# Kernel tuning notes

Hardware: AMD Instinct MI355X
Metric: run time of the kernel (lower is better)

## Reference

```python
import jax, jax.numpy as jnp
import numpy as np

N = 100000      # nodes
E = 1600000     # edges
F_IN = 512      # num_feat
HID = 128       # hidden dim (hardcoded in GNN)
ENC = 64        # encoder_dim
NCLS = 10       # num_classes
DOM = 40        # domain head hidden (hardcoded)


def setup_inputs() -> dict:
    key = jax.random.key(0)
    ks = jax.random.split(key, 16)
    def lin(k, fi, fo):
        kw, kb = jax.random.split(k)
        s = 1.0 / np.sqrt(fi)
        return (jax.random.uniform(kw, (fi, fo), jnp.float32, -s, s),
                jax.random.uniform(kb, (fo,), jnp.float32, -s, s))
    W1, b1 = lin(ks[0], F_IN, HID)
    W2, b2 = lin(ks[1], HID, ENC)
    att_w, att_b = lin(ks[2], ENC, 1)
    cls_w, cls_b = lin(ks[3], ENC, NCLS)
    dw1, db1 = lin(ks[4], ENC, DOM)
    dw2, db2 = lin(ks[5], DOM, 2)
    return {
        "x": jax.random.normal(ks[6], (N, F_IN), jnp.float32),
        "edge_index": jax.random.randint(ks[7], (2, E), 0, N, jnp.int64),
        "ppmi_edge_weight": jax.random.uniform(ks[8], (E,), jnp.float32, 0.01, 1.0),
        "rate": 1,
        "W1": W1, "b1": b1, "W2": W2, "b2": b2,
        "att_w": att_w, "att_b": att_b,
        "cls_w": cls_w, "cls_b": cls_b,
        "dw1": dw1, "db1": db1, "dw2": dw2, "db2": db2,
    }


def _edge_norm(src, dst, w):
    # symmetric normalization d^-1/2 * w * d^-1/2 (self-loops already included)
    deg = jax.ops.segment_sum(w, dst, num_segments=N)
    dinv = jnp.where(deg > 0, jax.lax.rsqrt(deg), 0.0)
    return dinv[src] * w * dinv[dst]


def _conv(h, W, b, src, dst, enorm):
    h = h @ W                                   # [N, out]
    msg = h[src] * enorm[:, None]               # [E+N, out] gather
    return jax.ops.segment_sum(msg, dst, num_segments=N) + b


def _encode(x, src, dst, enorm, W1, b1, W2, b2):
    h = jax.nn.relu(_conv(x, W1, b1, src, dst, enorm))  # dropout = identity (eval)
    return _conv(h, W2, b2, src, dst, enorm)


def reference(x, edge_index, ppmi_edge_weight, rate,
              W1, b1, W2, b2, att_w, att_b,
              cls_w, cls_b, dw1, db1, dw2, db2):
    loop = jnp.arange(N, dtype=edge_index.dtype)
    src = jnp.concatenate([edge_index[0], loop])
    dst = jnp.concatenate([edge_index[1], loop])
    ones_w = jnp.ones(src.shape[0], jnp.float32)
    ppmi_w = jnp.concatenate([ppmi_edge_weight, jnp.ones(N, jnp.float32)])

    gcn_norm = _edge_norm(src, dst, ones_w)
    ppmi_norm = _edge_norm(src, dst, ppmi_w)

    # both encoders share weights (base_model=self.encoder)
    g = _encode(x, src, dst, gcn_norm, W1, b1, W2, b2)    # [N, ENC]
    p = _encode(x, src, dst, ppmi_norm, W1, b1, W2, b2)   # [N, ENC]

    stacked = jnp.stack([g, p], axis=1)                   # [N, 2, ENC]
    logits = stacked @ att_w + att_b                      # [N, 2, 1]
    wts = jax.nn.softmax(logits, axis=1)
    emb = jnp.sum(stacked * wts, axis=1)                  # [N, ENC]

    class_predict = emb @ cls_w + cls_b
    r = jnp.float32(rate)
    # gradient reversal: identity fwd, -rate * grad bwd
    rev = jax.lax.stop_gradient((1.0 + r) * emb) - r * emb
    h = jax.nn.relu(rev @ dw1 + db1)                      # dropout = identity (eval)
    domain_predict = h @ dw2 + db2
    return emb, class_predict, domain_predict
```

## Files before the change

### kernel.cpp

```cpp
#include <hip/hip_runtime.h>
#include <math.h>
#include <stdint.h>

#define NND  100000
#define NED  1600000
#define FIN  512
#define HID  128
#define ENC  64
#define NCLS 10
#define DOM  40

#define SCAN_BS 256
#define NBS ((NND + SCAN_BS - 1) / SCAN_BS)

#define NGEMM 1563
#define NDEG  521
#define NPH1  (NGEMM + NDEG)

typedef __attribute__((ext_vector_type(8))) short short8v;
typedef __attribute__((ext_vector_type(8))) unsigned short ushort8v;
typedef __attribute__((ext_vector_type(4))) float f32x4;
typedef __attribute__((ext_vector_type(4))) unsigned int uint4v;


__device__ inline void split8(const float4 a, const float4 b,
                              short8v& hi, short8v& lo) {
  float f[8] = {a.x, a.y, a.z, a.w, b.x, b.y, b.z, b.w};
  uint4v H, L;
#pragma unroll
  for (int i = 0; i < 4; ++i) {
    unsigned int u0 = __float_as_uint(f[2 * i]);
    unsigned int u1 = __float_as_uint(f[2 * i + 1]);
    H[i] = (u0 >> 16) | (u1 & 0xffff0000u);
    float l0 = f[2 * i]     - __uint_as_float(u0 & 0xffff0000u);
    float l1 = f[2 * i + 1] - __uint_as_float(u1 & 0xffff0000u);
    L[i] = (__float_as_uint(l0) >> 16) | (__float_as_uint(l1) & 0xffff0000u);
  }
  hi = __builtin_bit_cast(short8v, H);
  lo = __builtin_bit_cast(short8v, L);
}

__device__ inline ushort f2bf_rne(float x) {
  unsigned int u = __float_as_uint(x);
  unsigned int r = u + 0x7fffu + ((u >> 16) & 1u);
  return (ushort)(r >> 16);
}

__device__ inline float bf2f(unsigned short v) {
  return __uint_as_float((unsigned int)v << 16);
}

__device__ inline void gload_lds16(const float* gp, float* lp) {
  __builtin_amdgcn_global_load_lds(
      (const __attribute__((address_space(1))) void*)gp,
      (__attribute__((address_space(3))) void*)lp, 16, 0, 0);
}


__global__ void k_prep(const float* __restrict__ W1, ushort* __restrict__ b1hi,
                       const float* __restrict__ W2,
                       ushort* __restrict__ b2hi, ushort* __restrict__ b2lo,
                       unsigned int* __restrict__ packed) {
  int id = blockIdx.x * 256 + threadIdx.x;
  if (id < NND) packed[id] = 0u;
  if (id < FIN * HID) {
    int k = id / HID, c = id % HID;
    size_t o = ((size_t)(k >> 3) * HID + c) * 8 + (k & 7);
    b1hi[o] = f2bf_rne(W1[id]);
  } else {
    int id2 = id - FIN * HID;
    if (id2 >= HID * ENC) return;
    int k = id2 / ENC, c = id2 % ENC;
    float x = W2[id2];
    unsigned int u = __float_as_uint(x);
    ushort h = (ushort)(u >> 16);
    float lo = x - __uint_as_float(u & 0xffff0000u);
    ushort l = (ushort)(__float_as_uint(lo) >> 16);
    size_t o = ((size_t)(k >> 3) * ENC + c) * 8 + (k & 7);
    b2hi[o] = h;
    b2lo[o] = l;
  }
}


__global__ __launch_bounds__(256, 4) void k_phase1(
    const float* __restrict__ A, const ushort* __restrict__ Bhi,
    ushort* __restrict__ C,
    const int* __restrict__ dst, const float* __restrict__ ppmi,
    unsigned int* __restrict__ packed, ushort* __restrict__ rank) {
  __shared__ float At[2][64 * 32];
  const int bi = blockIdx.x;
  const int tid = threadIdx.x;

  if ((bi & 3) == 0) {
    for (int e = (bi >> 2) * 256 + tid; e < NED; e += NDEG * 256) {
      int d = dst[e];
      unsigned int fx = (unsigned int)(ppmi[e] * 262144.0f + 0.5f);
      unsigned int v = (1u << 25) | fx;
      unsigned int old = atomicAdd(&packed[d], v);
      rank[e] = (ushort)(old >> 25);
    }
    return;
  }

  const int gb = bi - (bi >> 2) - 1;
  const int lane = tid & 63;
  const int w = tid >> 6;
  const int wr = w >> 1, wc = w & 1;
  const int g = lane >> 4;
  const int l16 = lane & 15;
  const int row_base = gb * 64;

  size_t srow[2]; int scol[2];
#pragma unroll
  for (int i = 0; i < 2; ++i) {
    int ee = i * 1024 + tid * 4;
    int r = ee >> 5;
    int chunk_lds = (ee >> 2) & 7;
    int chunk_g = chunk_lds ^ (r & 7);
    int rr = row_base + r; if (rr >= NND) rr = NND - 1;
    srow[i] = (size_t)rr * FIN;
    scol[i] = chunk_g * 4;
  }

  int coln[4];
#pragma unroll
  for (int n = 0; n < 4; ++n) coln[n] = wc * 64 + n * 16 + l16;
  int arow_l[2];
#pragma unroll
  for (int m = 0; m < 2; ++m) arow_l[m] = wr * 32 + m * 16 + l16;

  f32x4 acc[2][4] = {};

#pragma unroll
  for (int i = 0; i < 2; ++i)
    gload_lds16(A + srow[i] + 0 + scol[i], &At[0][i * 1024 + tid * 4]);
  __syncthreads();

  for (int t = 0; t < FIN / 32; ++t) {
    const int cur = t & 1;
    if (t + 1 < FIN / 32) {
      const int k0n = (t + 1) * 32;
#pragma unroll
      for (int i = 0; i < 2; ++i)
        gload_lds16(A + srow[i] + k0n + scol[i], &At[cur ^ 1][i * 1024 + tid * 4]);
    }

    short8v ah[2], al[2];
#pragma unroll
    for (int m = 0; m < 2; ++m) {
      int r = arow_l[m];
      int c0 = (((g * 2)     ^ (r & 7)) << 2);
      int c1 = (((g * 2 + 1) ^ (r & 7)) << 2);
      float4 a0 = *(const float4*)&At[cur][r * 32 + c0];
      float4 a1 = *(const float4*)&At[cur][r * 32 + c1];
      split8(a0, a1, ah[m], al[m]);
    }

    short8v bh[4];
    const int kc = t * 4 + g;
#pragma unroll
    for (int n = 0; n < 4; ++n)
      bh[n] = *(const short8v*)(Bhi + ((size_t)kc * HID + coln[n]) * 8);

#pragma unroll
    for (int m = 0; m < 2; ++m)
#pragma unroll
      for (int n = 0; n < 4; ++n) {
        acc[m][n] = __builtin_amdgcn_mfma_f32_16x16x32_bf16(ah[m], bh[n], acc[m][n], 0, 0, 0);
        acc[m][n] = __builtin_amdgcn_mfma_f32_16x16x32_bf16(al[m], bh[n], acc[m][n], 0, 0, 0);
      }

    __syncthreads();
  }

#pragma unroll
  for (int m = 0; m < 2; ++m)
#pragma unroll
    for (int i = 0; i < 4; ++i) {
      int r = row_base + wr * 32 + m * 16 + g * 4 + i;
      if (r < NND) {
#pragma unroll
        for (int n = 0; n < 4; ++n)
          C[(size_t)r * HID + coln[n]] = f2bf_rne(acc[m][n][i]);
      }
    }
}


__global__ void k_dinv_scan(const unsigned int* __restrict__ packed,
                            float* __restrict__ dinv_g, float* __restrict__ dinv_p,
                            int* __restrict__ psum) {
  __shared__ int s[SCAN_BS];
  int t = threadIdx.x, i = blockIdx.x * SCAN_BS + t;
  int cnt = 0;
  if (i < NND) {
    unsigned int pk = packed[i];
    cnt = (int)(pk >> 25);
    float dp = (float)(pk & 0x1FFFFFFu) * (1.0f / 262144.0f);
    dinv_g[i] = 1.0f / sqrtf((float)cnt + 1.0f);
    dinv_p[i] = 1.0f / sqrtf(dp + 1.0f);
  }
  s[t] = cnt;
  __syncthreads();
  for (int o = SCAN_BS / 2; o; o >>= 1) {
    if (t < o) s[t] += s[t + o];
    __syncthreads();
  }
  if (t == 0) psum[blockIdx.x] = s[0];
}

__global__ void k_scan_b(int* __restrict__ psum) {
  __shared__ int s[512];
  int t = threadIdx.x;
  int v = (t < NBS) ? psum[t] : 0;
  s[t] = v;
  __syncthreads();
  for (int o = 1; o < 512; o <<= 1) {
    int add = (t >= o) ? s[t - o] : 0;
    __syncthreads();
    s[t] += add;
    __syncthreads();
  }
  if (t < NBS) psum[t] = s[t] - v;
}

__global__ void k_scan_c(const unsigned int* __restrict__ packed,
                         const int* __restrict__ psum, int* __restrict__ row_ptr) {
  __shared__ int s[SCAN_BS];
  int t = threadIdx.x, i = blockIdx.x * SCAN_BS + t;
  int v = (i < NND) ? (int)(packed[i] >> 25) : 0;
  s[t] = v;
  __syncthreads();
  for (int o = 1; o < SCAN_BS; o <<= 1) {
    int add = (t >= o) ? s[t - o] : 0;
    __syncthreads();
    s[t] += add;
    __syncthreads();
  }
  if (i < NND) row_ptr[i] = psum[blockIdx.x] + s[t] - v;
  if (i == NND - 1) row_ptr[NND] = psum[blockIdx.x] + s[t];
}


__global__ void k_scatter(const int* __restrict__ src, const int* __restrict__ dst,
                          const float* __restrict__ ppmi,
                          const int* __restrict__ row_ptr, const ushort* __restrict__ rank,
                          const float* __restrict__ dinv_g, const float* __restrict__ dinv_p,
                          int2* __restrict__ csr) {
  int e = blockIdx.x * blockDim.x + threadIdx.x;
  if (e >= NED) return;
  int s = src[e], d = dst[e];
  int pos = row_ptr[d] + (int)rank[e];
  ushort gn = f2bf_rne(dinv_g[s] * dinv_g[d]);
  ushort pn = f2bf_rne(dinv_p[s] * ppmi[e] * dinv_p[d]);
  int2 rec;
  rec.x = s;
  rec.y = (int)gn | ((int)pn << 16);
  csr[pos] = rec;
}


__global__ __launch_bounds__(256, 4) void gemm2_split(
    const ushort* __restrict__ As, const ushort* __restrict__ Bhi,
    const ushort* __restrict__ Blo, ushort* __restrict__ C,
    int M, int K, int Nc) {
  const int lane = threadIdx.x & 63;
  const int w = threadIdx.x >> 6;
  const int g = lane >> 4;
  const int l16 = lane & 15;
  const int row_base = blockIdx.x * 128 + w * 32;

  size_t arow[2];
#pragma unroll
  for (int m = 0; m < 2; ++m) {
    int r = row_base + m * 16 + l16;
    if (r >= M) r = M - 1;
    arow[m] = (size_t)r * K;
  }
  int coln[4];
#pragma unroll
  for (int n = 0; n < 4; ++n) coln[n] = n * 16 + l16;

  f32x4 acc[2][4] = {};

  for (int k0 = 0; k0 < K; k0 += 32) {
    short8v ah[2];
#pragma unroll
    for (int m = 0; m < 2; ++m)
      ah[m] = *(const short8v*)(As + arow[m] + k0 + g * 8);
    short8v bh[4], bl[4];
    const int kc = (k0 >> 3) + g;
#pragma unroll
    for (int n = 0; n < 4; ++n) {
      size_t off = ((size_t)kc * Nc + coln[n]) * 8;
      bh[n] = *(const short8v*)(Bhi + off);
      bl[n] = *(const short8v*)(Blo + off);
    }
#pragma unroll
    for (int m = 0; m < 2; ++m)
#pragma unroll
      for (int n = 0; n < 4; ++n) {
        acc[m][n] = __builtin_amdgcn_mfma_f32_16x16x32_bf16(ah[m], bh[n], acc[m][n], 0, 0, 0);
        acc[m][n] = __builtin_amdgcn_mfma_f32_16x16x32_bf16(ah[m], bl[n], acc[m][n], 0, 0, 0);
      }
  }

#pragma unroll
  for (int m = 0; m < 2; ++m)
#pragma unroll
    for (int i = 0; i < 4; ++i) {
      int r = row_base + m * 16 + g * 4 + i;
      if (r < M) {
#pragma unroll
        for (int n = 0; n < 4; ++n) {
          int c = coln[n];
          size_t o = (r < NND) ? ((size_t)r * 128 + c)
                               : ((size_t)(r - NND) * 128 + 64 + c);
          C[o] = f2bf_rne(acc[m][n][i]);
        }
      }
    }
}


__global__ __launch_bounds__(256) void k_agg1(
    const ushort* __restrict__ hlinb, const int* __restrict__ row_ptr,
    const int2* __restrict__ csr,
    const float* __restrict__ dinv_g, const float* __restrict__ dinv_p,
    const float* __restrict__ b1, ushort* __restrict__ hhs) {
  int wid = (blockIdx.x * blockDim.x + threadIdx.x) >> 6;
  int lane = threadIdx.x & 63;
  if (wid >= NND) return;
  const int gp = lane >> 4;
  const int t  = lane & 15;
  float sg = dinv_g[wid]; sg *= sg;
  float sp = dinv_p[wid]; sp *= sp;

  float ag[8] = {}, ap[8] = {};
  if (gp == 0) {
    ushort8v v = *(const ushort8v*)(hlinb + (size_t)wid * HID + 8 * t);
#pragma unroll
    for (int i = 0; i < 8; ++i) {
      float f = bf2f(v[i]);
      ag[i] = f * sg; ap[i] = f * sp;
    }
  }
  int e0 = row_ptr[wid], e1 = row_ptr[wid + 1];
  int k = e0 + gp;
  if (k < e1) {
    int2 rec = csr[k];
    while (true) {
      int kn = k + 4;
      int2 nrec = csr[kn < e1 ? kn : k];
      float wg = bf2f((ushort)(rec.y & 0xffff));
      float wp = bf2f((ushort)((unsigned)rec.y >> 16));
      ushort8v u = *(const ushort8v*)(hlinb + (size_t)rec.x * HID + 8 * t);
#pragma unroll
      for (int i = 0; i < 8; ++i) {
        float f = bf2f(u[i]);
        ag[i] = fmaf(f, wg, ag[i]);
        ap[i] = fmaf(f, wp, ap[i]);
      }
      if (kn >= e1) break;
      k = kn; rec = nrec;
    }
  }
#pragma unroll
  for (int i = 0; i < 8; ++i) {
    ag[i] += __shfl_xor(ag[i], 32); ap[i] += __shfl_xor(ap[i], 32);
    ag[i] += __shfl_xor(ag[i], 16); ap[i] += __shfl_xor(ap[i], 16);
  }

  float bb[8];
  *(float4*)&bb[0] = *(const float4*)(b1 + 8 * t);
  *(float4*)&bb[4] = *(const float4*)(b1 + 8 * t + 4);
  if (gp == 0 || gp == 2) {
    ushort8v outv;
#pragma unroll
    for (int i = 0; i < 8; ++i) {
      float v = (gp == 0) ? fmaxf(ag[i] + bb[i], 0.f) : fmaxf(ap[i] + bb[i], 0.f);
      outv[i] = f2bf_rne(v);
    }
    size_t row = (gp == 0) ? (size_t)wid : (size_t)(NND + wid);
    *(ushort8v*)(hhs + row * HID + 8 * t) = outv;
  }
}


__global__ __launch_bounds__(256) void k_agg2(
    const ushort* __restrict__ h2b, const int* __restrict__ row_ptr,
    const int2* __restrict__ csr,
    const float* __restrict__ dinv_g, const float* __restrict__ dinv_p,
    const float* __restrict__ b2, const float* __restrict__ att_w,
    const float* __restrict__ att_b, float* __restrict__ out_emb) {
  int wid = (blockIdx.x * blockDim.x + threadIdx.x) >> 6;
  int lane = threadIdx.x & 63;
  if (wid >= NND) return;
  const int gp = lane >> 4;
  const int t  = lane & 15;
  const int br = t >> 3;
  const int f0 = (t & 7) * 8;
  float sg = dinv_g[wid]; sg *= sg;
  float sp = dinv_p[wid]; sp *= sp;
  const float sw = br ? sp : sg;

  float acc[8] = {};
  if (gp == 0) {
    ushort8v v = *(const ushort8v*)(h2b + (size_t)wid * 128 + 8 * t);
#pragma unroll
    for (int i = 0; i < 8; ++i) acc[i] = bf2f(v[i]) * sw;
  }
  int e0 = row_ptr[wid], e1 = row_ptr[wid + 1];
  int k = e0 + gp;
  if (k < e1) {
    int2 rec = csr[k];
    while (true) {
      int kn = k + 4;
      int2 nrec = csr[kn < e1 ? kn : k];
      float w = br ? bf2f((ushort)((unsigned)rec.y >> 16))
                   : bf2f((ushort)(rec.y & 0xffff));
      ushort8v u = *(const ushort8v*)(h2b + (size_t)rec.x * 128 + 8 * t);
#pragma unroll
      for (int i = 0; i < 8; ++i) acc[i] = fmaf(bf2f(u[i]), w, acc[i]);
      if (kn >= e1) break;
      k = kn; rec = nrec;
    }
  }
#pragma unroll
  for (int i = 0; i < 8; ++i) {
    acc[i] += __shfl_xor(acc[i], 32);
    acc[i] += __shfl_xor(acc[i], 16);
  }

  float bb[8];
  *(float4*)&bb[0] = *(const float4*)(b2 + f0);
  *(float4*)&bb[4] = *(const float4*)(b2 + f0 + 4);
  float v[8];
#pragma unroll
  for (int i = 0; i < 8; ++i) v[i] = acc[i] + bb[i];

  float aw[8];
  *(float4*)&aw[0] = *(const float4*)(att_w + f0);
  *(float4*)&aw[4] = *(const float4*)(att_w + f0 + 4);
  float part = 0.f;
#pragma unroll
  for (int i = 0; i < 8; ++i) part = fmaf(v[i], aw[i], part);
  part += __shfl_xor(part, 4);
  part += __shfl_xor(part, 2);
  part += __shfl_xor(part, 1);
  float other = __shfl_xor(part, 8);
  float ab = att_b[0];
  float lg = (br ? other : part) + ab;
  float lp = (br ? part : other) + ab;
  float mx = fmaxf(lg, lp);
  float eg = expf(lg - mx), ep2 = expf(lp - mx);
  float wsm = eg / (eg + ep2);

  float ov[8];
#pragma unroll
  for (int i = 0; i < 8; ++i) ov[i] = __shfl_xor(v[i], 8);
  if (gp == 0 && br == 0) {
    float4* dst = (float4*)(out_emb + (size_t)wid * 64 + f0);
    float4 o0, o1;
    o0.x = wsm * v[0] + (1.f - wsm) * ov[0];
    o0.y = wsm * v[1] + (1.f - wsm) * ov[1];
    o0.z = wsm * v[2] + (1.f - wsm) * ov[2];
    o0.w = wsm * v[3] + (1.f - wsm) * ov[3];
    o1.x = wsm * v[4] + (1.f - wsm) * ov[4];
    o1.y = wsm * v[5] + (1.f - wsm) * ov[5];
    o1.z = wsm * v[6] + (1.f - wsm) * ov[6];
    o1.w = wsm * v[7] + (1.f - wsm) * ov[7];
    dst[0] = o0;
    dst[1] = o1;
  }
}


__global__ __launch_bounds__(128) void k_head(
    const float* __restrict__ emb,
    const float* __restrict__ cls_w, const float* __restrict__ cls_b,
    const float* __restrict__ dw1, const float* __restrict__ db1,
    const float* __restrict__ dw2, const float* __restrict__ db2,
    float* __restrict__ out_cls, float* __restrict__ out_dom) {
  __shared__ float se[128 * 65];
  const int t = threadIdx.x;
  const int base = blockIdx.x * 128;
  for (int c = 0; c < 64; ++c) {
    int idx = c * 128 + t;
    int nl = idx >> 6, k = idx & 63;
    size_t g = (size_t)base * ENC + idx;
    float v = (g < (size_t)NND * ENC) ? emb[g] : 0.f;
    se[nl * 65 + k] = v;
  }
  __syncthreads();

  int node = base + t;
  float c[NCLS], hd[DOM];
#pragma unroll
  for (int j = 0; j < NCLS; ++j) c[j] = cls_b[j];
#pragma unroll
  for (int j = 0; j < DOM; ++j) hd[j] = db1[j];

  for (int k = 0; k < ENC; ++k) {
    float ev = se[t * 65 + k];
#pragma unroll
    for (int j = 0; j < NCLS; ++j) c[j] += ev * cls_w[k * NCLS + j];
#pragma unroll
    for (int j = 0; j < DOM; ++j) hd[j] += ev * dw1[k * DOM + j];
  }
  float d0 = db2[0], d1 = db2[1];
#pragma unroll
  for (int j = 0; j < DOM; ++j) {
    float hv = fmaxf(hd[j], 0.f);
    d0 += hv * dw2[j * 2];
    d1 += hv * dw2[j * 2 + 1];
  }
  if (node < NND) {
#pragma unroll
    for (int j = 0; j < NCLS; ++j) out_cls[(size_t)node * NCLS + j] = c[j];
    out_dom[(size_t)node * 2]     = d0;
    out_dom[(size_t)node * 2 + 1] = d1;
  }
}


extern "C" void kernel_launch(void* const* d_in, const int* in_sizes, int n_in,
                              void* d_out, int out_size, void* d_ws, size_t ws_size,
                              hipStream_t stream) {
  const float* x     = (const float*)d_in[0];
  const int*   ei    = (const int*)d_in[1];
  const float* ppmi  = (const float*)d_in[2];
  const float* W1    = (const float*)d_in[4];
  const float* b1    = (const float*)d_in[5];
  const float* W2    = (const float*)d_in[6];
  const float* b2    = (const float*)d_in[7];
  const float* att_w = (const float*)d_in[8];
  const float* att_b = (const float*)d_in[9];
  const float* cls_w = (const float*)d_in[10];
  const float* cls_b = (const float*)d_in[11];
  const float* dw1   = (const float*)d_in[12];
  const float* db1   = (const float*)d_in[13];
  const float* dw2   = (const float*)d_in[14];
  const float* db2   = (const float*)d_in[15];

  const int* src = ei;
  const int* dst = ei + NED;

  uintptr_t p = (uintptr_t)d_ws;
  auto alloc = [&](size_t bytes) -> void* {
    void* r = (void*)p;
    p += (bytes + 255) & ~(size_t)255;
    return r;
  };
  unsigned int* packed = (unsigned int*)alloc((size_t)NND * 4);
  ushort* rank    = (ushort*)alloc((size_t)NED * 2);
  int*    row_ptr = (int*)   alloc((size_t)(NND + 1) * 4);
  int*    psum    = (int*)   alloc((size_t)NBS * 4);
  float*  dinv_g  = (float*) alloc((size_t)NND * 4);
  float*  dinv_p  = (float*) alloc((size_t)NND * 4);
  int2*   csr     = (int2*)  alloc((size_t)NED * 8);
  ushort* b1hi    = (ushort*)alloc((size_t)FIN * HID * 2);
  ushort* b2hi    = (ushort*)alloc((size_t)HID * ENC * 2);
  ushort* b2lo    = (ushort*)alloc((size_t)HID * ENC * 2);
  ushort* h2b     = (ushort*)alloc((size_t)NND * HID * 2);
  ushort* hhs     = (ushort*)alloc((size_t)2 * NND * HID * 2);

  float* out_emb = (float*)d_out;
  float* out_cls = (float*)d_out + (size_t)NND * ENC;
  float* out_dom = (float*)d_out + (size_t)NND * (ENC + NCLS);

  ushort* h_linb = (ushort*)d_out;

  k_prep<<<(NND + 255) / 256, 256, 0, stream>>>(W1, b1hi, W2, b2hi, b2lo,
                                                packed);

  k_phase1<<<NPH1, 256, 0, stream>>>(x, b1hi, h_linb, dst, ppmi, packed, rank);

  k_dinv_scan<<<NBS, SCAN_BS, 0, stream>>>(packed, dinv_g, dinv_p, psum);
  k_scan_b<<<1, 512, 0, stream>>>(psum);
  k_scan_c<<<NBS, SCAN_BS, 0, stream>>>(packed, psum, row_ptr);
  k_scatter<<<NED / 256, 256, 0, stream>>>(src, dst, ppmi, row_ptr, rank,
                                           dinv_g, dinv_p, csr);

  k_agg1<<<(NND * 64) / 256, 256, 0, stream>>>(h_linb, row_ptr, csr,
                                               dinv_g, dinv_p, b1, hhs);
  gemm2_split<<<(2 * NND + 127) / 128, 256, 0, stream>>>(
      hhs, b2hi, b2lo, h2b, 2 * NND, HID, ENC);
  k_agg2<<<(NND * 64) / 256, 256, 0, stream>>>(h2b, row_ptr, csr,
                                               dinv_g, dinv_p, b2, att_w, att_b, out_emb);

  k_head<<<(NND + 127) / 128, 128, 0, stream>>>(out_emb, cls_w, cls_b, dw1, db1,
                                                dw2, db2, out_cls, out_dom);
}
```

Before: 379.2 us.

## Replace three-kernel CSR scan with single-pass atomic block allocation

New measurement: 459.2 us. +21.1%, slower.

```diff
diff --git a/kernel.cpp b/kernel.cpp
--- a/kernel.cpp
+++ b/kernel.cpp
@@ -60,8 +60,9 @@
 __global__ void k_prep(const float* __restrict__ W1, ushort* __restrict__ b1hi,
                        const float* __restrict__ W2,
                        ushort* __restrict__ b2hi, ushort* __restrict__ b2lo,
-                       unsigned int* __restrict__ packed) {
+                       unsigned int* __restrict__ packed, int* __restrict__ cursor) {
   int id = blockIdx.x * 256 + threadIdx.x;
+  if (id == 0) *cursor = 0;
   if (id < NND) packed[id] = 0u;
   if (id < FIN * HID) {
     int k = id / HID, c = id % HID;
@@ -83,7 +84,7 @@
 }
 
 
-__global__ __launch_bounds__(256, 4) void k_phase1(
+__global__ __launch_bounds__(256, 8) void k_phase1(
     const float* __restrict__ A, const ushort* __restrict__ Bhi,
     ushort* __restrict__ C,
     const int* __restrict__ dst, const float* __restrict__ ppmi,
@@ -188,10 +189,11 @@
 }
 
 
-__global__ void k_dinv_scan(const unsigned int* __restrict__ packed,
-                            float* __restrict__ dinv_g, float* __restrict__ dinv_p,
-                            int* __restrict__ psum) {
+__global__ void k_dinv_alloc(const unsigned int* __restrict__ packed,
+                             float* __restrict__ dinv_g, float* __restrict__ dinv_p,
+                             int* __restrict__ row_ptr, int* __restrict__ cursor) {
   __shared__ int s[SCAN_BS];
+  __shared__ int base;
   int t = threadIdx.x, i = blockIdx.x * SCAN_BS + t;
   int cnt = 0;
   if (i < NND) {
@@ -203,43 +205,15 @@
   }
   s[t] = cnt;
   __syncthreads();
-  for (int o = SCAN_BS / 2; o; o >>= 1) {
-    if (t < o) s[t] += s[t + o];
-    __syncthreads();
-  }
-  if (t == 0) psum[blockIdx.x] = s[0];
-}
-
-__global__ void k_scan_b(int* __restrict__ psum) {
-  __shared__ int s[512];
-  int t = threadIdx.x;
-  int v = (t < NBS) ? psum[t] : 0;
-  s[t] = v;
-  __syncthreads();
-  for (int o = 1; o < 512; o <<= 1) {
-    int add = (t >= o) ? s[t - o] : 0;
-    __syncthreads();
-    s[t] += add;
-    __syncthreads();
-  }
-  if (t < NBS) psum[t] = s[t] - v;
-}
-
-__global__ void k_scan_c(const unsigned int* __restrict__ packed,
-                         const int* __restrict__ psum, int* __restrict__ row_ptr) {
-  __shared__ int s[SCAN_BS];
-  int t = threadIdx.x, i = blockIdx.x * SCAN_BS + t;
-  int v = (i < NND) ? (int)(packed[i] >> 25) : 0;
-  s[t] = v;
-  __syncthreads();
   for (int o = 1; o < SCAN_BS; o <<= 1) {
     int add = (t >= o) ? s[t - o] : 0;
     __syncthreads();
     s[t] += add;
     __syncthreads();
   }
-  if (i < NND) row_ptr[i] = psum[blockIdx.x] + s[t] - v;
-  if (i == NND - 1) row_ptr[NND] = psum[blockIdx.x] + s[t];
+  if (t == SCAN_BS - 1) base = atomicAdd(cursor, s[t]);
+  __syncthreads();
+  if (i < NND) row_ptr[i] = base + s[t] - cnt;
 }
 
 
@@ -326,7 +300,7 @@
 
 __global__ __launch_bounds__(256) void k_agg1(
     const ushort* __restrict__ hlinb, const int* __restrict__ row_ptr,
-    const int2* __restrict__ csr,
+    const unsigned int* __restrict__ packed, const int2* __restrict__ csr,
     const float* __restrict__ dinv_g, const float* __restrict__ dinv_p,
     const float* __restrict__ b1, ushort* __restrict__ hhs) {
   int wid = (blockIdx.x * blockDim.x + threadIdx.x) >> 6;
@@ -346,7 +320,8 @@
       ag[i] = f * sg; ap[i] = f * sp;
     }
   }
-  int e0 = row_ptr[wid], e1 = row_ptr[wid + 1];
+  int e0 = row_ptr[wid];
+  int e1 = e0 + (int)(packed[wid] >> 25);
   int k = e0 + gp;
   if (k < e1) {
     int2 rec = csr[k];
@@ -390,7 +365,7 @@
 
 __global__ __launch_bounds__(256) void k_agg2(
     const ushort* __restrict__ h2b, const int* __restrict__ row_ptr,
-    const int2* __restrict__ csr,
+    const unsigned int* __restrict__ packed, const int2* __restrict__ csr,
     const float* __restrict__ dinv_g, const float* __restrict__ dinv_p,
     const float* __restrict__ b2, const float* __restrict__ att_w,
     const float* __restrict__ att_b, float* __restrict__ out_emb) {
@@ -411,7 +386,8 @@
 #pragma unroll
     for (int i = 0; i < 8; ++i) acc[i] = bf2f(v[i]) * sw;
   }
-  int e0 = row_ptr[wid], e1 = row_ptr[wid + 1];
+  int e0 = row_ptr[wid];
+  int e1 = e0 + (int)(packed[wid] >> 25);
   int k = e0 + gp;
   if (k < e1) {
     int2 rec = csr[k];
@@ -554,9 +530,9 @@
     return r;
   };
   unsigned int* packed = (unsigned int*)alloc((size_t)NND * 4);
+  int*    cursor  = (int*)   alloc(256);
   ushort* rank    = (ushort*)alloc((size_t)NED * 2);
   int*    row_ptr = (int*)   alloc((size_t)(NND + 1) * 4);
-  int*    psum    = (int*)   alloc((size_t)NBS * 4);
   float*  dinv_g  = (float*) alloc((size_t)NND * 4);
   float*  dinv_p  = (float*) alloc((size_t)NND * 4);
   int2*   csr     = (int2*)  alloc((size_t)NED * 8);
@@ -573,21 +549,19 @@
   ushort* h_linb = (ushort*)d_out;
 
   k_prep<<<(NND + 255) / 256, 256, 0, stream>>>(W1, b1hi, W2, b2hi, b2lo,
-                                                packed);
+                                                packed, cursor);
 
   k_phase1<<<NPH1, 256, 0, stream>>>(x, b1hi, h_linb, dst, ppmi, packed, rank);
 
-  k_dinv_scan<<<NBS, SCAN_BS, 0, stream>>>(packed, dinv_g, dinv_p, psum);
-  k_scan_b<<<1, 512, 0, stream>>>(psum);
-  k_scan_c<<<NBS, SCAN_BS, 0, stream>>>(packed, psum, row_ptr);
+  k_dinv_alloc<<<NBS, SCAN_BS, 0, stream>>>(packed, dinv_g, dinv_p, row_ptr, cursor);
   k_scatter<<<NED / 256, 256, 0, stream>>>(src, dst, ppmi, row_ptr, rank,
                                            dinv_g, dinv_p, csr);
 
-  k_agg1<<<(NND * 64) / 256, 256, 0, stream>>>(h_linb, row_ptr, csr,
+  k_agg1<<<(NND * 64) / 256, 256, 0, stream>>>(h_linb, row_ptr, packed, csr,
                                                dinv_g, dinv_p, b1, hhs);
   gemm2_split<<<(2 * NND + 127) / 128, 256, 0, stream>>>(
       hhs, b2hi, b2lo, h2b, 2 * NND, HID, ENC);
-  k_agg2<<<(NND * 64) / 256, 256, 0, stream>>>(h2b, row_ptr, csr,
+  k_agg2<<<(NND * 64) / 256, 256, 0, stream>>>(h2b, row_ptr, packed, csr,
                                                dinv_g, dinv_p, b2, att_w, att_b, out_emb);
 
   k_head<<<(NND + 127) / 128, 128, 0, stream>>>(out_emb, cls_w, cls_b, dw1, db1,
```
